# Optimization experiments

Measured on AMD Instinct MI355X. Metric: run time of the kernel, lower is better.

Reference implementation:

```python
import jax, jax.numpy as jnp
import numpy as np

N = 100000        # nodes
E = 3200000       # edges
IN = 256          # in_feats
H = 8             # num_heads
O = 64            # out_feats
F = 64            # edge_feats
T = 8             # num_etypes

def setup_inputs() -> dict:
    key = jax.random.key(0)
    ks = jax.random.split(key, 10)
    return {
        "feat": jax.random.normal(ks[0], (N, IN), jnp.float32) * 0.1,
        "etype": jax.random.randint(ks[1], (E,), 0, T, jnp.int32),
        "src": jax.random.randint(ks[2], (E,), 0, N, jnp.int32),
        "dst": jax.random.randint(ks[3], (E,), 0, N, jnp.int32),
        "W_fc": jax.random.normal(ks[4], (IN, H * O), jnp.float32) * (1.0 / np.sqrt(IN)),
        "edge_emb": jax.random.normal(ks[5], (T, F), jnp.float32),
        "W_e": jax.random.normal(ks[6], (F, H * F), jnp.float32) * (1.0 / np.sqrt(F)),
        "attn_l": jax.random.normal(ks[7], (H, O), jnp.float32) * 0.1,
        "attn_r": jax.random.normal(ks[8], (H, O), jnp.float32) * 0.1,
        "attn_e": jax.random.normal(ks[9], (H, F), jnp.float32) * 0.1,
    }

def reference(feat, etype, src, dst, W_fc, edge_emb, W_e, attn_l, attn_r, attn_e):
    n = feat.shape[0]
    # node projection + per-head attention logits
    h = (feat @ W_fc).reshape(n, H, O)                      # [N,H,O]
    el = jnp.einsum('nho,ho->nh', h, attn_l)                # [N,H]
    er = jnp.einsum('nho,ho->nh', h, attn_r)                # [N,H]
    # edge-type embedding -> projection -> logit (project the tiny table once, then gather)
    emb_proj = (edge_emb @ W_e).reshape(T, H, F)            # [T,H,F]
    ee = jnp.einsum('thf,hf->th', emb_proj, attn_e)[etype]  # [E,H]
    # u_add_v + edge bias, then ReLU (module's "leaky_relu" is nn.ReLU())
    e = jax.nn.relu(el[src] + er[dst] + ee)                 # [E,H]
    # segment softmax grouped by destination node
    m = jax.ops.segment_max(e, dst, num_segments=n)         # [N,H]
    ex = jnp.exp(e - m[dst])                                # [E,H]
    s = jax.ops.segment_sum(ex, dst, num_segments=n)        # [N,H]
    return ex / s[dst]                                      # [E,H]
```

## Files before the change

### kernel.cpp

```cpp
#include <hip/hip_runtime.h>
#include <math.h>

#define NN 100000
#define NE 3200000
#define INF_ 256
#define NH 8
#define OF 64
#define EF 64
#define NT 8

#define BSH 7
#define BNODES 128
#define NB 782
#define CAPB 4608
#define SPLIT 2
#define CHUNK 2304
#define EPB 4096

static constexpr size_t WS_AT      = 0;
static constexpr size_t WS_EE      = 4096;
static constexpr size_t WS_EL      = 4160;
static constexpr size_t WS_ERS     = WS_EL + (size_t)NN * 8;
static constexpr size_t WS_CCNT    = WS_ERS + (size_t)NN * 16;
static constexpr size_t WS_PART    = WS_CCNT + NB + 2;
static constexpr size_t WS_PARTIAL = WS_PART + (size_t)NB * CAPB;

__global__ __launch_bounds__(256) void k_prep_A(const float* __restrict__ W_fc,
                                                const float* __restrict__ attn_l,
                                                const float* __restrict__ attn_r,
                                                float* __restrict__ At,
                                                unsigned* __restrict__ ccnt) {
    int t = blockIdx.x * 256 + threadIdx.x;
    if (t < NB) ccnt[t] = 0u;
    int c = t >> 8;
    int i = t & 255;
    int h = c & 7;
    const float* attn = (c < 8) ? attn_l : attn_r;
    const float* wrow = W_fc + (size_t)i * (NH * OF) + h * OF;
    const float* arow = attn + h * OF;
    float acc = 0.f;
#pragma unroll 8
    for (int o = 0; o < OF; ++o) acc += wrow[o] * arow[o];
    At[c * INF_ + i] = acc;
}

__global__ __launch_bounds__(512) void k_prep_ee(const float* __restrict__ edge_emb,
                                                 const float* __restrict__ W_e,
                                                 const float* __restrict__ attn_e,
                                                 float* __restrict__ ee_tab) {
    __shared__ float B[EF][NH];
    int t = threadIdx.x;
    int g = t >> 3, h = t & 7;
    const float* wrow = W_e + (size_t)g * (NH * EF) + h * EF;
    const float* arow = attn_e + h * EF;
    float acc = 0.f;
#pragma unroll 8
    for (int f = 0; f < EF; ++f) acc += wrow[f] * arow[f];
    B[g][h] = acc;
    __syncthreads();
    if (t < NT * NH) {
        int tt = t >> 3, hh = t & 7;
        float a = 0.f;
#pragma unroll 8
        for (int g2 = 0; g2 < EF; ++g2) a += edge_emb[tt * EF + g2] * B[g2][hh];
        ee_tab[tt * NH + hh] = a;
    }
}

__global__ __launch_bounds__(256) void k_node(const float* __restrict__ feat,
                                              const float* __restrict__ At,
                                              float* __restrict__ el,
                                              float* __restrict__ ers) {
    int n = blockIdx.x * 256 + threadIdx.x;
    if (n >= NN) return;
    const float4* f4 = (const float4*)(feat + (size_t)n * INF_);
    const float4* A4 = (const float4*)At;
    float acc[16];
#pragma unroll
    for (int c = 0; c < 16; ++c) acc[c] = 0.f;
    for (int iq = 0; iq < INF_ / 4; ++iq) {
        float4 f = f4[iq];
#pragma unroll
        for (int c = 0; c < 16; ++c) {
            float4 a = A4[c * 64 + iq];
            acc[c] += f.x * a.x + f.y * a.y + f.z * a.z + f.w * a.w;
        }
    }
    float4* e4 = (float4*)(el + (size_t)n * 8);
    e4[0] = make_float4(acc[0], acc[1], acc[2], acc[3]);
    e4[1] = make_float4(acc[4], acc[5], acc[6], acc[7]);
    float4* r4 = (float4*)(ers + (size_t)n * 16);
    r4[0] = make_float4(acc[8], acc[9], acc[10], acc[11]);
    r4[1] = make_float4(acc[12], acc[13], acc[14], acc[15]);
}

__global__ __launch_bounds__(256) void k_partition(const int* __restrict__ src,
                                                   const int* __restrict__ dst,
                                                   const int* __restrict__ etype,
                                                   unsigned* __restrict__ ccnt,
                                                   unsigned* __restrict__ part) {
    __shared__ unsigned hist[NB];
    __shared__ unsigned cursor[NB];
    int tid = threadIdx.x;
    size_t base = (size_t)blockIdx.x * EPB;
    unsigned long long rc[16];
    for (int i = tid; i < NB; i += 256) hist[i] = 0u;
    __syncthreads();
#pragma unroll
    for (int k = 0; k < 16; ++k) {
        size_t j = base + (size_t)k * 256 + tid;
        if (j < NE) {
            int dj = dst[j];
            rc[k] = (unsigned long long)(unsigned)src[j]
                  | ((unsigned long long)(unsigned)etype[j] << 17)
                  | ((unsigned long long)(unsigned)dj << 20);
            atomicAdd(&hist[dj >> BSH], 1u);
        } else rc[k] = ~0ull;
    }
    __syncthreads();
    for (int i = tid; i < NB; i += 256) {
        unsigned h = hist[i];
        cursor[i] = h ? atomicAdd(ccnt + i, h) : 0u;
    }
    __syncthreads();
#pragma unroll
    for (int k = 0; k < 16; ++k) {
        if (rc[k] == ~0ull) continue;
        int dj = (int)(rc[k] >> 20);
        int b = dj >> BSH;
        unsigned pos = atomicAdd(&cursor[b], 1u);
        if (pos < CAPB)
            part[(size_t)b * CAPB + pos] =
                (unsigned)(rc[k] & 0xFFFFFull) | ((unsigned)(dj & (BNODES - 1)) << 20);
    }
}

__global__ __launch_bounds__(256) void k_bucket_sum(const unsigned* __restrict__ part,
                                                    const unsigned* __restrict__ ccnt,
                                                    const float* __restrict__ el,
                                                    const float* __restrict__ ers,
                                                    const float* __restrict__ ee_tab,
                                                    float* __restrict__ partial) {
    __shared__ float sbin[BNODES * 9];
    __shared__ float er_l[BNODES * 9];
    __shared__ float ee_l[NT * NH];
    int bs = blockIdx.x;
    int b = bs >> 1, c = bs & 1;
    int tid = threadIdx.x;
    int e_sub = tid >> 3, h = tid & 7;
    int n0 = b << BSH;
    int nn = NN - n0; if (nn > BNODES) nn = BNODES;

    for (int i = tid; i < BNODES * 9; i += 256) sbin[i] = 0.f;
    if (tid < NT * NH) ee_l[tid] = ee_tab[tid];
    for (int i = tid; i < nn * NH; i += 256) {
        int nl = i >> 3, hh = i & 7;
        er_l[nl * 9 + hh] = ers[(size_t)(n0 + nl) * 16 + hh];
    }
    __syncthreads();

    unsigned cnt = ccnt[b]; if (cnt > CAPB) cnt = CAPB;
    unsigned hi = (unsigned)(c + 1) * CHUNK; if (hi > cnt) hi = cnt;
    const unsigned* pp = part + (size_t)b * CAPB;
    for (unsigned e = (unsigned)c * CHUNK + e_sub; e < hi; e += 32) {
        unsigned rec = pp[e];
        int sj = (int)(rec & 0x1FFFFu);
        int et = (int)((rec >> 17) & 7u);
        int dl = (int)((rec >> 20) & (BNODES - 1));
        float v = el[(size_t)sj * 8 + h] + er_l[dl * 9 + h] + ee_l[et * NH + h];
        atomicAdd(&sbin[dl * 9 + h], expf(fmaxf(v, 0.f)));
    }
    __syncthreads();
    float* po = partial + ((size_t)b * SPLIT + c) * (BNODES * NH);
    for (int i = tid; i < nn * NH; i += 256)
        po[i] = sbin[(i >> 3) * 9 + (i & 7)];
}

__global__ __launch_bounds__(256) void k_reduce(const float* __restrict__ partial,
                                                float* __restrict__ ers) {
    int t = blockIdx.x * 256 + threadIdx.x;
    if (t >= NN * NH) return;
    int n = t >> 3, h = t & 7;
    int b = n >> BSH, nl = n & (BNODES - 1);
    const float* pa = partial + (size_t)b * SPLIT * (BNODES * NH);
    ers[(size_t)n * 16 + 8 + h] = pa[nl * NH + h] + pa[BNODES * NH + nl * NH + h];
}

__global__ __launch_bounds__(256) void k_edge_out(const int* __restrict__ src,
                                                  const int* __restrict__ dst,
                                                  const int* __restrict__ etype,
                                                  const float* __restrict__ el,
                                                  const float* __restrict__ ers,
                                                  const float* __restrict__ ee_tab,
                                                  float* __restrict__ out) {
    int j = blockIdx.x * 256 + threadIdx.x;
    if (j >= NE) return;
    int sj = src[j], dj = dst[j], tj = etype[j];
    const float4* el4 = (const float4*)(el + (size_t)sj * 8);
    const float4* E   = (const float4*)(ers + (size_t)dj * 16);
    const float4* ee4 = (const float4*)(ee_tab + tj * NH);
    float4 l0 = el4[0], l1 = el4[1];
    float4 r0 = E[0], r1 = E[1];
    float4 s0 = E[2], s1 = E[3];
    float4 e0 = ee4[0], e1 = ee4[1];
    float4 o0, o1;
    o0.x = expf(fmaxf(l0.x + r0.x + e0.x, 0.f)) / s0.x;
    o0.y = expf(fmaxf(l0.y + r0.y + e0.y, 0.f)) / s0.y;
    o0.z = expf(fmaxf(l0.z + r0.z + e0.z, 0.f)) / s0.z;
    o0.w = expf(fmaxf(l0.w + r0.w + e0.w, 0.f)) / s0.w;
    o1.x = expf(fmaxf(l1.x + r1.x + e1.x, 0.f)) / s1.x;
    o1.y = expf(fmaxf(l1.y + r1.y + e1.y, 0.f)) / s1.y;
    o1.z = expf(fmaxf(l1.z + r1.z + e1.z, 0.f)) / s1.z;
    o1.w = expf(fmaxf(l1.w + r1.w + e1.w, 0.f)) / s1.w;
    float4* o4 = (float4*)(out + (size_t)j * NH);
    o4[0] = o0;
    o4[1] = o1;
}

extern "C" void kernel_launch(void* const* d_in, const int* in_sizes, int n_in,
                              void* d_out, int out_size, void* d_ws, size_t ws_size,
                              hipStream_t stream) {
    const float* feat     = (const float*)d_in[0];
    const int*   etype    = (const int*)d_in[1];
    const int*   src      = (const int*)d_in[2];
    const int*   dst      = (const int*)d_in[3];
    const float* W_fc     = (const float*)d_in[4];
    const float* edge_emb = (const float*)d_in[5];
    const float* W_e      = (const float*)d_in[6];
    const float* attn_l   = (const float*)d_in[7];
    const float* attn_r   = (const float*)d_in[8];
    const float* attn_e   = (const float*)d_in[9];

    float*    ws      = (float*)d_ws;
    float*    At      = ws + WS_AT;
    float*    ee_tab  = ws + WS_EE;
    float*    el      = ws + WS_EL;
    float*    ers     = ws + WS_ERS;
    unsigned* ccnt    = (unsigned*)(ws + WS_CCNT);
    unsigned* part    = (unsigned*)(ws + WS_PART);
    float*    partial = ws + WS_PARTIAL;
    float*    out     = (float*)d_out;

    hipLaunchKernelGGL(k_prep_A, dim3(16), dim3(256), 0, stream, W_fc, attn_l, attn_r, At, ccnt);
    hipLaunchKernelGGL(k_prep_ee, dim3(1), dim3(512), 0, stream, edge_emb, W_e, attn_e, ee_tab);
    hipLaunchKernelGGL(k_node, dim3((NN + 255) / 256), dim3(256), 0, stream, feat, At, el, ers);
    hipLaunchKernelGGL(k_partition, dim3((NE + EPB - 1) / EPB), dim3(256), 0, stream,
                       src, dst, etype, ccnt, part);
    hipLaunchKernelGGL(k_bucket_sum, dim3(NB * SPLIT), dim3(256), 0, stream,
                       part, ccnt, el, ers, ee_tab, partial);
    hipLaunchKernelGGL(k_reduce, dim3((NN * NH + 255) / 256), dim3(256), 0, stream,
                       partial, ers);
    hipLaunchKernelGGL(k_edge_out, dim3((NE + 255) / 256), dim3(256), 0, stream,
                       src, dst, etype, el, ers, ee_tab, out);
}
```

Before: 560.5 us.

## Vectorize and software-pipeline bucket sum, double edges per thread in edge_out

The bucket-sum kernel now has each thread load four packed records at once with a uint4 load and prefetch the next group while the current one is processed. The el gathers are hoisted ahead of the shared-memory atomics to raise memory-level parallelism. The edge output kernel handles two edges per thread with int2 index loads, and the partition kernel processes twice as many edges per block. The intent is fewer, wider memory transactions and more loads in flight, paid for with higher register use and lower occupancy.

Result: no change. 566.9 us (+1.1%).

```diff
diff --git a/kernel.cpp b/kernel.cpp
--- a/kernel.cpp
+++ b/kernel.cpp
@@ -15,7 +15,7 @@
 #define CAPB 4608
 #define SPLIT 2
 #define CHUNK 2304
-#define EPB 4096
+#define EPB 8192
 
 static constexpr size_t WS_AT      = 0;
 static constexpr size_t WS_EE      = 4096;
@@ -103,11 +103,11 @@
     __shared__ unsigned cursor[NB];
     int tid = threadIdx.x;
     size_t base = (size_t)blockIdx.x * EPB;
-    unsigned long long rc[16];
+    unsigned long long rc[32];
     for (int i = tid; i < NB; i += 256) hist[i] = 0u;
     __syncthreads();
 #pragma unroll
-    for (int k = 0; k < 16; ++k) {
+    for (int k = 0; k < 32; ++k) {
         size_t j = base + (size_t)k * 256 + tid;
         if (j < NE) {
             int dj = dst[j];
@@ -124,7 +124,7 @@
     }
     __syncthreads();
 #pragma unroll
-    for (int k = 0; k < 16; ++k) {
+    for (int k = 0; k < 32; ++k) {
         if (rc[k] == ~0ull) continue;
         int dj = (int)(rc[k] >> 20);
         int b = dj >> BSH;
@@ -147,7 +147,8 @@
     int bs = blockIdx.x;
     int b = bs >> 1, c = bs & 1;
     int tid = threadIdx.x;
-    int e_sub = tid >> 3, h = tid & 7;
+    int eq = tid >> 3;
+    int h  = tid & 7;
     int n0 = b << BSH;
     int nn = NN - n0; if (nn > BNODES) nn = BNODES;
 
@@ -160,15 +161,49 @@
     __syncthreads();
 
     unsigned cnt = ccnt[b]; if (cnt > CAPB) cnt = CAPB;
-    unsigned hi = (unsigned)(c + 1) * CHUNK; if (hi > cnt) hi = cnt;
+    unsigned lo = (unsigned)c * CHUNK;
+    unsigned hi = lo + CHUNK; if (hi > cnt) hi = cnt;
     const unsigned* pp = part + (size_t)b * CAPB;
-    for (unsigned e = (unsigned)c * CHUNK + e_sub; e < hi; e += 32) {
-        unsigned rec = pp[e];
-        int sj = (int)(rec & 0x1FFFFu);
-        int et = (int)((rec >> 17) & 7u);
-        int dl = (int)((rec >> 20) & (BNODES - 1));
-        float v = el[(size_t)sj * 8 + h] + er_l[dl * 9 + h] + ee_l[et * NH + h];
-        atomicAdd(&sbin[dl * 9 + h], expf(fmaxf(v, 0.f)));
+
+    if (lo < hi) {
+        auto load4 = [&](unsigned base_e) {
+            unsigned e = base_e + 4u * eq;
+            uint4 r = make_uint4(0u, 0u, 0u, 0u);
+            if (e + 3 < hi) r = *(const uint4*)(pp + e);
+            else {
+                if (e     < hi) r.x = pp[e];
+                if (e + 1 < hi) r.y = pp[e + 1];
+                if (e + 2 < hi) r.z = pp[e + 2];
+                if (e + 3 < hi) r.w = pp[e + 3];
+            }
+            return r;
+        };
+        uint4 r = load4(lo);
+        for (unsigned base = lo; base < hi; base += 128) {
+            uint4 rn;
+            bool more = (base + 128 < hi);
+            if (more) rn = load4(base + 128);
+            unsigned e = base + 4u * eq;
+            unsigned recs[4] = {r.x, r.y, r.z, r.w};
+            float vv[4];
+#pragma unroll
+            for (int k = 0; k < 4; ++k) {
+                if (e + k < hi) {
+                    int sj = (int)(recs[k] & 0x1FFFFu);
+                    vv[k] = el[(size_t)sj * 8 + h];
+                }
+            }
+#pragma unroll
+            for (int k = 0; k < 4; ++k) {
+                if (e + k < hi) {
+                    int et = (int)((recs[k] >> 17) & 7u);
+                    int dl = (int)((recs[k] >> 20) & (BNODES - 1));
+                    float v = vv[k] + er_l[dl * 9 + h] + ee_l[et * NH + h];
+                    atomicAdd(&sbin[dl * 9 + h], expf(fmaxf(v, 0.f)));
+                }
+            }
+            r = rn;
+        }
     }
     __syncthreads();
     float* po = partial + ((size_t)b * SPLIT + c) * (BNODES * NH);
@@ -193,28 +228,44 @@
                                                   const float* __restrict__ ers,
                                                   const float* __restrict__ ee_tab,
                                                   float* __restrict__ out) {
-    int j = blockIdx.x * 256 + threadIdx.x;
-    if (j >= NE) return;
-    int sj = src[j], dj = dst[j], tj = etype[j];
-    const float4* el4 = (const float4*)(el + (size_t)sj * 8);
-    const float4* E   = (const float4*)(ers + (size_t)dj * 16);
-    const float4* ee4 = (const float4*)(ee_tab + tj * NH);
-    float4 l0 = el4[0], l1 = el4[1];
-    float4 r0 = E[0], r1 = E[1];
-    float4 s0 = E[2], s1 = E[3];
-    float4 e0 = ee4[0], e1 = ee4[1];
-    float4 o0, o1;
-    o0.x = expf(fmaxf(l0.x + r0.x + e0.x, 0.f)) / s0.x;
-    o0.y = expf(fmaxf(l0.y + r0.y + e0.y, 0.f)) / s0.y;
-    o0.z = expf(fmaxf(l0.z + r0.z + e0.z, 0.f)) / s0.z;
-    o0.w = expf(fmaxf(l0.w + r0.w + e0.w, 0.f)) / s0.w;
-    o1.x = expf(fmaxf(l1.x + r1.x + e1.x, 0.f)) / s1.x;
-    o1.y = expf(fmaxf(l1.y + r1.y + e1.y, 0.f)) / s1.y;
-    o1.z = expf(fmaxf(l1.z + r1.z + e1.z, 0.f)) / s1.z;
-    o1.w = expf(fmaxf(l1.w + r1.w + e1.w, 0.f)) / s1.w;
-    float4* o4 = (float4*)(out + (size_t)j * NH);
-    o4[0] = o0;
-    o4[1] = o1;
+    int j0 = (blockIdx.x * 256 + threadIdx.x) * 2;
+    if (j0 + 1 >= NE) {
+        if (j0 >= NE) return;
+    }
+    int2 sj = *(const int2*)(src + j0);
+    int2 dj = *(const int2*)(dst + j0);
+    int2 tj = *(const int2*)(etype + j0);
+    const float4* elA = (const float4*)(el + (size_t)sj.x * 8);
+    const float4* elB = (const float4*)(el + (size_t)sj.y * 8);
+    const float4* EA  = (const float4*)(ers + (size_t)dj.x * 16);
+    const float4* EB  = (const float4*)(ers + (size_t)dj.y * 16);
+    float4 la0 = elA[0], la1 = elA[1];
+    float4 lb0 = elB[0], lb1 = elB[1];
+    float4 ra0 = EA[0], ra1 = EA[1], sa0 = EA[2], sa1 = EA[3];
+    float4 rb0 = EB[0], rb1 = EB[1], sb0 = EB[2], sb1 = EB[3];
+    const float4* eeA = (const float4*)(ee_tab + tj.x * NH);
+    const float4* eeB = (const float4*)(ee_tab + tj.y * NH);
+    float4 ea0 = eeA[0], ea1 = eeA[1];
+    float4 eb0 = eeB[0], eb1 = eeB[1];
+    float4 o0, o1, o2, o3;
+    o0.x = expf(fmaxf(la0.x + ra0.x + ea0.x, 0.f)) / sa0.x;
+    o0.y = expf(fmaxf(la0.y + ra0.y + ea0.y, 0.f)) / sa0.y;
+    o0.z = expf(fmaxf(la0.z + ra0.z + ea0.z, 0.f)) / sa0.z;
+    o0.w = expf(fmaxf(la0.w + ra0.w + ea0.w, 0.f)) / sa0.w;
+    o1.x = expf(fmaxf(la1.x + ra1.x + ea1.x, 0.f)) / sa1.x;
+    o1.y = expf(fmaxf(la1.y + ra1.y + ea1.y, 0.f)) / sa1.y;
+    o1.z = expf(fmaxf(la1.z + ra1.z + ea1.z, 0.f)) / sa1.z;
+    o1.w = expf(fmaxf(la1.w + ra1.w + ea1.w, 0.f)) / sa1.w;
+    o2.x = expf(fmaxf(lb0.x + rb0.x + eb0.x, 0.f)) / sb0.x;
+    o2.y = expf(fmaxf(lb0.y + rb0.y + eb0.y, 0.f)) / sb0.y;
+    o2.z = expf(fmaxf(lb0.z + rb0.z + eb0.z, 0.f)) / sb0.z;
+    o2.w = expf(fmaxf(lb0.w + rb0.w + eb0.w, 0.f)) / sb0.w;
+    o3.x = expf(fmaxf(lb1.x + rb1.x + eb1.x, 0.f)) / sb1.x;
+    o3.y = expf(fmaxf(lb1.y + rb1.y + eb1.y, 0.f)) / sb1.y;
+    o3.z = expf(fmaxf(lb1.z + rb1.z + eb1.z, 0.f)) / sb1.z;
+    o3.w = expf(fmaxf(lb1.w + rb1.w + eb1.w, 0.f)) / sb1.w;
+    float4* o4 = (float4*)(out + (size_t)j0 * NH);
+    o4[0] = o0; o4[1] = o1; o4[2] = o2; o4[3] = o3;
 }
 
 extern "C" void kernel_launch(void* const* d_in, const int* in_sizes, int n_in,
@@ -250,6 +301,6 @@
                        part, ccnt, el, ers, ee_tab, partial);
     hipLaunchKernelGGL(k_reduce, dim3((NN * NH + 255) / 256), dim3(256), 0, stream,
                        partial, ers);
-    hipLaunchKernelGGL(k_edge_out, dim3((NE + 255) / 256), dim3(256), 0, stream,
+    hipLaunchKernelGGL(k_edge_out, dim3(NE / 512, 1, 1), dim3(256), 0, stream,
                        src, dst, etype, el, ers, ee_tab, out);
 }
```
